# Optimization experiments

Measured on AMD Instinct MI355X. Metric: run time of the kernel, lower is better.

The kernel has to match this reference:

```python
import jax, jax.numpy as jnp
import numpy as np

B, S, E, H, L, NQ, FFN, V, C = 16, 2048, 256, 4, 2, 8, 512, 50257, 2
DK = E // H  # wires per attention head


def _pos_encoding(seq_len, dim):
    pos = jnp.arange(seq_len, dtype=jnp.float32)[:, None]
    div = jnp.exp(jnp.arange(0, dim, 2, dtype=jnp.float32) * (-np.log(10000.0) / dim))
    pe = jnp.zeros((seq_len, dim), dtype=jnp.float32)
    pe = pe.at[:, 0::2].set(jnp.sin(pos * div))
    pe = pe.at[:, 1::2].set(jnp.cos(pos * div))
    return pe


def _layernorm(x, g, b, eps=1e-5):
    m = x.mean(-1, keepdims=True)
    v = ((x - m) ** 2).mean(-1, keepdims=True)
    return (x - m) / jnp.sqrt(v + eps) * g + b


def setup_inputs() -> dict:
    key = jax.random.key(0)
    ks = jax.random.split(key, 9)
    f = lambda k, shape, s: jax.random.normal(k, shape, dtype=jnp.float32) * s
    return {
        "tokens": jax.random.randint(ks[0], (B, S), 0, V),
        "embed": f(ks[1], (V, E), 0.02),
        "attn_theta": f(ks[2], (L, DK), 1.0),
        "combine_w": f(ks[3], (L, E, E), 0.05),
        "combine_b": jnp.zeros((L, E), jnp.float32),
        "ffn_theta": f(ks[4], (L, NQ), 1.0),
        "lin1_w": f(ks[5], (L, NQ, FFN), 0.1),
        "lin1_b": jnp.zeros((L, FFN), jnp.float32),
        "lin2_w": f(ks[6], (L, FFN, E), 0.05),
        "lin2_b": jnp.zeros((L, E), jnp.float32),
        "ln1_g": jnp.ones((L, E), jnp.float32),
        "ln1_b": jnp.zeros((L, E), jnp.float32),
        "ln2_g": jnp.ones((L, E), jnp.float32),
        "ln2_b": jnp.zeros((L, E), jnp.float32),
        "cls_w": f(ks[7], (E, C), 0.05),
        "cls_b": jnp.zeros((C,), jnp.float32),
    }


def reference(tokens, embed, attn_theta, combine_w, combine_b, ffn_theta,
              lin1_w, lin1_b, lin2_w, lin2_b, ln1_g, ln1_b, ln2_g, ln2_b,
              cls_w, cls_b):
    # token embedding + sinusoidal positional encoding
    x = embed[tokens] + _pos_encoding(S, E)[None]  # [B,S,E]
    for l in range(L):
        # QuantumAttention: per-head RX-encode(x) then trainable RX(theta),
        # PauliZ expectation => cos(x + theta); same theta shared across heads,
        # head split/merge preserves feature layout => tile theta over heads.
        theta = jnp.tile(attn_theta[l], H)  # [E]
        attn = jnp.einsum('bse,ef->bsf', jnp.cos(x + theta), combine_w[l]) + combine_b[l]
        x = _layernorm(x + attn, ln1_g[l], ln1_b[l])
        # FeedForwardQuantum: RX-encode first NQ features, trainable RY(theta),
        # PauliZ expectation => cos(x) * cos(theta)
        q = jnp.cos(x[..., :NQ]) * jnp.cos(ffn_theta[l])  # [B,S,NQ]
        h = jax.nn.relu(jnp.einsum('bsn,nf->bsf', q, lin1_w[l]) + lin1_b[l])
        ffn = jnp.einsum('bsf,fe->bse', h, lin2_w[l]) + lin2_b[l]
        x = _layernorm(x + ffn, ln2_g[l], ln2_b[l])
    pooled = x.mean(axis=1)  # [B,E]
    return pooled @ cls_w + cls_b  # [B,C] logits
```

## Files before the change

kernel.cpp:

```cpp
#include <hip/hip_runtime.h>
#include <cstdint>
#include <cstddef>

#define SEQ   2048
#define EDIM  256
#define FFND  512
#define NBATCH 16
#define XLD   264

typedef unsigned short u16;
typedef __attribute__((ext_vector_type(8))) __bf16 bf16x8;
typedef __attribute__((ext_vector_type(4))) float f32x4;

__device__ __forceinline__ float bf2f(u16 u) {
  union { unsigned int w; float f; } v; v.w = ((unsigned int)u) << 16; return v.f;
}
__device__ __forceinline__ u16 f2bf(float f) {
  union { float f; unsigned int w; } v; v.f = f;
  unsigned int r = v.w + 0x7fffu + ((v.w >> 16) & 1u);
  return (u16)(r >> 16);
}
__device__ __forceinline__ float fast_cos(float x) {
  float r = x * 0.15915494309189535f;
  r = r - floorf(r);
  return __builtin_amdgcn_cosf(r);
}
__device__ __forceinline__ void unpack8(bf16x8 v, float* o) {
  const u16* p = (const u16*)&v;
  #pragma unroll
  for (int j = 0; j < 8; ++j) o[j] = bf2f(p[j]);
}

__global__ void sniff_kernel(const void* embed, int* flag) {
  int t = threadIdx.x;
  const u16* p = (const u16*)embed;
  int c = 0;
  #pragma unroll
  for (int j = 0; j < 8; ++j) {
    u16 v = p[t * 8 + j];
    int e = (v >> 7) & 0xff;
    c += (e > 128) ? 1 : 0;
  }
  #pragma unroll
  for (int d = 1; d < 64; d <<= 1) c += __shfl_xor(c, d);
  if (t == 0) *flag = (c > 64) ? 1 : 0;
}

struct CanonArgs { const void* p[14]; };

__global__ void canon_kernel(CanonArgs a, const int* __restrict__ flag, u16* __restrict__ dst) {
  const int off[15] = {0, 128, 131200, 131712, 131728, 139920, 140944, 403088,
                       403600, 404112, 404624, 405136, 405648, 406160, 406162};
  int i = blockIdx.x * 256 + threadIdx.x;
  if (i >= 406162) return;
  int isf32 = *flag;
  int s = 0;
  #pragma unroll
  for (int k = 0; k < 13; ++k) s += (i >= off[k + 1]) ? 1 : 0;
  int j = i - off[s];
  u16 v = isf32 ? f2bf(((const float*)a.p[s])[j]) : ((const u16*)a.p[s])[j];
  dst[i] = v;
}

__global__ void prep_kernel(const u16* __restrict__ cw, const u16* __restrict__ l2,
                            u16* __restrict__ cwT, u16* __restrict__ l2T) {
  int id = blockIdx.x * 256 + threadIdx.x;
  if (id < 2 * 256 * 256) {
    int l = id >> 16, rem = id & 65535;
    int kc = rem >> 11, n = (rem >> 3) & 255, kj = rem & 7;
    cwT[id] = cw[l * 65536 + (kc * 8 + kj) * 256 + n];
  } else {
    int j = id - 131072;
    if (j < 2 * 512 * 256) {
      int l = j >> 17, rem = j & 131071;
      int kc = rem >> 11, n = (rem >> 3) & 255, kj = rem & 7;
      l2T[j] = l2[l * 131072 + (kc * 8 + kj) * 256 + n];
    }
  }
}

__launch_bounds__(256, 2)
__global__ void mega_kernel(const int* __restrict__ tokens, const void* __restrict__ embed,
                            const int* __restrict__ flag, const u16* __restrict__ canon,
                            const u16* __restrict__ cwT, const u16* __restrict__ l2T,
                            float* __restrict__ pooled) {
  __shared__ u16 xt[64 * XLD];
  __shared__ union {
    struct { u16 Bt[256 * 64]; u16 At[64 * 64]; u16 qs[64 * 8]; } k;
    struct { float2 sstat[64][5]; float2 sms[64]; } ln;
  } sh;
  __shared__ u16 thL[64];

  const int tid = threadIdx.x;
  const int wave = tid >> 6, lane = tid & 63;
  const int fr = lane & 15, fq = lane >> 4;
  const int m0 = blockIdx.x * 64;
  const int isf32 = *flag;

  int cols[4];
  #pragma unroll
  for (int ni = 0; ni < 4; ++ni) cols[ni] = wave * 64 + ni * 16 + fr;

  {
    const float c0 = 9.210340371976184f / 128.f;
    const float inv2pi = 0.15915494309189535f;
    #pragma unroll
    for (int it = 0; it < 8; ++it) {
      int c = it * 256 + tid;
      int r = c >> 5, e8 = c & 31;
      int tok = tokens[m0 + r];
      float ev[8];
      if (isf32) {
        const float* ep = (const float*)embed + (size_t)tok * EDIM + e8 * 8;
        float4 a = *(const float4*)ep, b = *(const float4*)(ep + 4);
        ev[0]=a.x; ev[1]=a.y; ev[2]=a.z; ev[3]=a.w; ev[4]=b.x; ev[5]=b.y; ev[6]=b.z; ev[7]=b.w;
      } else {
        const u16* ep = (const u16*)embed + (size_t)tok * EDIM + e8 * 8;
        uint4 v = *(const uint4*)ep;
        unpack8(*(const bf16x8*)&v, ev);
      }
      int s = (m0 + r) & (SEQ - 1);
      u16 o[8];
      #pragma unroll
      for (int j = 0; j < 8; ++j) {
        int e = e8 * 8 + j, i = e >> 1;
        float rev = (float)s * (__expf(-(float)i * c0) * inv2pi);
        rev = rev - floorf(rev);
        float pe = (e & 1) ? __builtin_amdgcn_cosf(rev) : __builtin_amdgcn_sinf(rev);
        o[j] = f2bf(ev[j] + pe);
      }
      *(uint4*)(xt + r * XLD + e8 * 8) = *(const uint4*)o;
    }
  }
  __syncthreads();

  f32x4 acc[4][4];

  auto mfma_step = [&]() {
    const bf16x8* Av = (const bf16x8*)sh.k.At;
    const bf16x8* Bv = (const bf16x8*)sh.k.Bt;
    #pragma unroll
    for (int ks = 0; ks < 2; ++ks) {
      const int kc = ks * 4 + fq;
      bf16x8 af[4], bfv[4];
      #pragma unroll
      for (int mi = 0; mi < 4; ++mi) af[mi] = Av[kc * 64 + ((mi * 16 + fr) ^ kc)];
      #pragma unroll
      for (int ni = 0; ni < 4; ++ni) bfv[ni] = Bv[kc * 256 + cols[ni]];
      #pragma unroll
      for (int mi = 0; mi < 4; ++mi)
        #pragma unroll
        for (int ni = 0; ni < 4; ++ni)
          acc[mi][ni] = __builtin_amdgcn_mfma_f32_16x16x32_bf16(af[mi], bfv[ni], acc[mi][ni], 0, 0, 0);
    }
  };

  auto epilogue = [&](const u16* bias, const u16* gamma, const u16* beta) {
    float bcol[4];
    #pragma unroll
    for (int ni = 0; ni < 4; ++ni) bcol[ni] = bf2f(bias[cols[ni]]);
    #pragma unroll
    for (int mi = 0; mi < 4; ++mi)
      #pragma unroll
      for (int rg = 0; rg < 4; ++rg) {
        int lrow = mi * 16 + fq * 4 + rg;
        #pragma unroll
        for (int ni = 0; ni < 4; ++ni)
          acc[mi][ni][rg] += bf2f(xt[lrow * XLD + cols[ni]]) + bcol[ni];
      }
    float sr[4][4], sq[4][4];
    #pragma unroll
    for (int mi = 0; mi < 4; ++mi)
      #pragma unroll
      for (int rg = 0; rg < 4; ++rg) {
        float a = 0.f, b = 0.f;
        #pragma unroll
        for (int ni = 0; ni < 4; ++ni) { float t2 = acc[mi][ni][rg]; a += t2; b += t2 * t2; }
        sr[mi][rg] = a; sq[mi][rg] = b;
      }
    #pragma unroll
    for (int d = 1; d < 16; d <<= 1)
      #pragma unroll
      for (int mi = 0; mi < 4; ++mi)
        #pragma unroll
        for (int rg = 0; rg < 4; ++rg) {
          sr[mi][rg] += __shfl_xor(sr[mi][rg], d);
          sq[mi][rg] += __shfl_xor(sq[mi][rg], d);
        }
    if (fr == 0) {
      #pragma unroll
      for (int mi = 0; mi < 4; ++mi)
        #pragma unroll
        for (int rg = 0; rg < 4; ++rg)
          sh.ln.sstat[mi * 16 + fq * 4 + rg][wave] = float2{sr[mi][rg], sq[mi][rg]};
    }
    __syncthreads();
    if (tid < 64) {
      float s = 0.f, s2 = 0.f;
      #pragma unroll
      for (int w = 0; w < 4; ++w) { float2 p = sh.ln.sstat[tid][w]; s += p.x; s2 += p.y; }
      float mean = s * (1.f / 256.f);
      float var = fmaxf(s2 * (1.f / 256.f) - mean * mean, 0.f);
      sh.ln.sms[tid] = float2{mean, rsqrtf(var + 1e-5f)};
    }
    __syncthreads();
    float gcol[4], btc[4];
    #pragma unroll
    for (int ni = 0; ni < 4; ++ni) { gcol[ni] = bf2f(gamma[cols[ni]]); btc[ni] = bf2f(beta[cols[ni]]); }
    #pragma unroll
    for (int mi = 0; mi < 4; ++mi)
      #pragma unroll
      for (int rg = 0; rg < 4; ++rg) {
        int lrow = mi * 16 + fq * 4 + rg;
        float2 ms = sh.ln.sms[lrow];
        #pragma unroll
        for (int ni = 0; ni < 4; ++ni) {
          float o = (acc[mi][ni][rg] - ms.x) * ms.y * gcol[ni] + btc[ni];
          xt[lrow * XLD + cols[ni]] = f2bf(o);
        }
      }
    __syncthreads();
  };

  for (int l = 0; l < 2; ++l) {
    if (tid < 8) ((uint4*)thL)[tid] = ((const uint4*)(canon + l * 64))[tid];
    __syncthreads();
    #pragma unroll
    for (int i = 0; i < 4; ++i)
      #pragma unroll
      for (int j = 0; j < 4; ++j) acc[i][j] = {0.f, 0.f, 0.f, 0.f};
    {
      const u16* Bbase = cwT + l * 65536;
      for (int k0 = 0; k0 < 256; k0 += 64) {
        const u16* bsrc = Bbase + (k0 >> 3) * 2048;
        #pragma unroll
        for (int it = 0; it < 8; ++it) {
          int c = tid + it * 256;
          __builtin_amdgcn_global_load_lds(
              (const __attribute__((address_space(1))) void*)(bsrc + (size_t)c * 8),
              (__attribute__((address_space(3))) void*)(sh.k.Bt + c * 8), 16, 0, 0);
        }
        #pragma unroll
        for (int it = 0; it < 2; ++it) {
          int c = it * 256 + tid;
          int f8 = c >> 6, r = c & 63;
          uint4 g = *(const uint4*)(xt + r * XLD + k0 + f8 * 8);
          u16* gp = (u16*)&g;
          #pragma unroll
          for (int j = 0; j < 8; ++j)
            gp[j] = f2bf(fast_cos(bf2f(gp[j]) + bf2f(thL[f8 * 8 + j])));
          ((uint4*)sh.k.At)[f8 * 64 + (r ^ f8)] = g;
        }
        __syncthreads();
        mfma_step();
        __syncthreads();
      }
    }
    epilogue(canon + 131200 + l * 256, canon + 403600 + l * 256, canon + 404112 + l * 256);

    #pragma unroll
    for (int rep = 0; rep < 2; ++rep) {
      int idx = tid + rep * 256;
      int r = idx >> 3, n = idx & 7;
      float cth = fast_cos(bf2f(canon[131712 + l * 8 + n]));
      sh.k.qs[r * 8 + n] = f2bf(fast_cos(bf2f(xt[r * XLD + n])) * cth);
    }
    __syncthreads();

    #pragma unroll
    for (int i = 0; i < 4; ++i)
      #pragma unroll
      for (int j = 0; j < 4; ++j) acc[i][j] = {0.f, 0.f, 0.f, 0.f};
    {
      const u16* B2 = l2T + l * 131072;
      const u16* w1 = canon + 131728 + l * 4096;
      const u16* b1 = canon + 139920 + l * 512;
      for (int k0 = 0; k0 < 512; k0 += 64) {
        const u16* bsrc = B2 + (k0 >> 3) * 2048;
        #pragma unroll
        for (int it = 0; it < 8; ++it) {
          int c = tid + it * 256;
          __builtin_amdgcn_global_load_lds(
              (const __attribute__((address_space(1))) void*)(bsrc + (size_t)c * 8),
              (__attribute__((address_space(3))) void*)(sh.k.Bt + c * 8), 16, 0, 0);
        }
        #pragma unroll
        for (int it = 0; it < 2; ++it) {
          int c = it * 256 + tid;
          int kc = c >> 6, r = c & 63;
          int cc = (k0 >> 3) + kc;
          float qf[8], hv[8];
          unpack8(((const bf16x8*)sh.k.qs)[r], qf);
          { uint4 bv = *(const uint4*)(b1 + cc * 8); unpack8(*(const bf16x8*)&bv, hv); }
          #pragma unroll
          for (int n = 0; n < 8; ++n) {
            uint4 wv = *(const uint4*)(w1 + n * 512 + cc * 8);
            float wf[8];
            unpack8(*(const bf16x8*)&wv, wf);
            #pragma unroll
            for (int j = 0; j < 8; ++j) hv[j] += qf[n] * wf[j];
          }
          uint4 g; u16* gp = (u16*)&g;
          #pragma unroll
          for (int j = 0; j < 8; ++j) gp[j] = f2bf(fmaxf(hv[j], 0.f));
          ((uint4*)sh.k.At)[kc * 64 + (r ^ kc)] = g;
        }
        __syncthreads();
        mfma_step();
        __syncthreads();
      }
    }
    epilogue(canon + 403088 + l * 256, canon + 404624 + l * 256, canon + 405136 + l * 256);
  }

  {
    float s = 0.f;
    #pragma unroll 8
    for (int r = 0; r < 64; ++r) s += bf2f(xt[r * XLD + tid]);
    atomicAdd(&pooled[(m0 >> 11) * EDIM + tid], s);
  }
}

__global__ void logits_kernel(const float* __restrict__ pooled, const u16* __restrict__ clsw,
                              const u16* __restrict__ clsb, const int* __restrict__ flag,
                              void* __restrict__ out) {
  int t = threadIdx.x;
  int b = t >> 4, sub = t & 15;
  float a0 = 0.f, a1 = 0.f;
  #pragma unroll
  for (int j = 0; j < 16; ++j) {
    int e = sub * 16 + j;
    float p = pooled[b * 256 + e];
    a0 += p * bf2f(clsw[e * 2 + 0]);
    a1 += p * bf2f(clsw[e * 2 + 1]);
  }
  #pragma unroll
  for (int d = 1; d < 16; d <<= 1) {
    a0 += __shfl_xor(a0, d);
    a1 += __shfl_xor(a1, d);
  }
  if (sub == 0) {
    float o0 = a0 * (1.f / 2048.f) + bf2f(clsb[0]);
    float o1 = a1 * (1.f / 2048.f) + bf2f(clsb[1]);
    if (*flag) {
      ((float*)out)[b * 2 + 0] = o0; ((float*)out)[b * 2 + 1] = o1;
    } else {
      ((u16*)out)[b * 2 + 0] = f2bf(o0); ((u16*)out)[b * 2 + 1] = f2bf(o1);
    }
  }
}

extern "C" void kernel_launch(void* const* d_in, const int* in_sizes, int n_in,
                              void* d_out, int out_size, void* d_ws, size_t ws_size,
                              hipStream_t stream) {
  const int* tokens = (const int*)d_in[0];

  char* ws = (char*)d_ws;
  u16*   canon  = (u16*)(ws + 0);
  u16*   cwT    = (u16*)(ws + 1048576);
  u16*   l2T    = (u16*)(ws + 1310720);
  float* pooled = (float*)(ws + 1835008);
  int*   flag   = (int*)(ws + 1851392);

  sniff_kernel<<<1, 64, 0, stream>>>(d_in[1], flag);

  CanonArgs ca;
  for (int i = 0; i < 14; ++i) ca.p[i] = d_in[i + 2];
  canon_kernel<<<1587, 256, 0, stream>>>(ca, flag, canon);

  prep_kernel<<<1536, 256, 0, stream>>>(canon + 128, canon + 140944, cwT, l2T);

  hipMemsetAsync(pooled, 0, NBATCH * EDIM * sizeof(float), stream);

  mega_kernel<<<512, 256, 0, stream>>>(tokens, d_in[1], flag, canon, cwT, l2T, pooled);

  logits_kernel<<<1, 256, 0, stream>>>(pooled, canon + 405648, canon + 406160, flag, d_out);
}
```

Before: 215.4 us.

## Run FFN lin1 on MFMA, precompute positional table, simplify LayerNorm reduction

The scalar FMA loop that computed the lin1 hidden activations is replaced by bf16 MFMA with zero-padded K, using q fragments and a transposed lin1 weight produced in the prep kernel. The positional encoding is now computed once by a separate kernel into a workspace table and read in the embedding stage, which removes the per-element exp and sin/cos work. The LayerNorm row statistics now write per-lane partials to shared memory instead of doing shuffle reductions, and one thread per row sums them. In exchange the MFMA wastes three quarters of its K lanes, the scattered 16-bit stores into At may cause bank conflicts, and the positional table adds 2 MB of global reads.

```diff
diff --git a/kernel.cpp b/kernel.cpp
--- a/kernel.cpp
+++ b/kernel.cpp
@@ -63,31 +63,47 @@
 }
 
 __global__ void prep_kernel(const u16* __restrict__ cw, const u16* __restrict__ l2,
-                            u16* __restrict__ cwT, u16* __restrict__ l2T) {
+                            const u16* __restrict__ w1, u16* __restrict__ cwT,
+                            u16* __restrict__ l2T, u16* __restrict__ w1T) {
   int id = blockIdx.x * 256 + threadIdx.x;
-  if (id < 2 * 256 * 256) {
+  if (id < 131072) {
     int l = id >> 16, rem = id & 65535;
     int kc = rem >> 11, n = (rem >> 3) & 255, kj = rem & 7;
     cwT[id] = cw[l * 65536 + (kc * 8 + kj) * 256 + n];
-  } else {
+  } else if (id < 393216) {
     int j = id - 131072;
-    if (j < 2 * 512 * 256) {
-      int l = j >> 17, rem = j & 131071;
-      int kc = rem >> 11, n = (rem >> 3) & 255, kj = rem & 7;
-      l2T[j] = l2[l * 131072 + (kc * 8 + kj) * 256 + n];
-    }
-  }
+    int l = j >> 17, rem = j & 131071;
+    int kc = rem >> 11, n = (rem >> 3) & 255, kj = rem & 7;
+    l2T[j] = l2[l * 131072 + (kc * 8 + kj) * 256 + n];
+  } else if (id < 401408) {
+    int j = id - 393216;
+    int l = j >> 12, rem = j & 4095;
+    int c = rem >> 3, n = rem & 7;
+    w1T[j] = w1[l * 4096 + n * 512 + c];
+  }
+}
+
+__global__ void pe_kernel(float* __restrict__ pe) {
+  int id = blockIdx.x * 256 + threadIdx.x;
+  int s = id >> 8, e = id & 255;
+  const float c0 = 9.210340371976184f / 128.f;
+  const float inv2pi = 0.15915494309189535f;
+  int i = e >> 1;
+  float rev = (float)s * (__expf(-(float)i * c0) * inv2pi);
+  rev = rev - floorf(rev);
+  pe[id] = (e & 1) ? __builtin_amdgcn_cosf(rev) : __builtin_amdgcn_sinf(rev);
 }
 
 __launch_bounds__(256, 2)
 __global__ void mega_kernel(const int* __restrict__ tokens, const void* __restrict__ embed,
                             const int* __restrict__ flag, const u16* __restrict__ canon,
                             const u16* __restrict__ cwT, const u16* __restrict__ l2T,
+                            const u16* __restrict__ w1T, const float* __restrict__ pe,
                             float* __restrict__ pooled) {
   __shared__ u16 xt[64 * XLD];
   __shared__ union {
     struct { u16 Bt[256 * 64]; u16 At[64 * 64]; u16 qs[64 * 8]; } k;
-    struct { float2 sstat[64][5]; float2 sms[64]; } ln;
+    struct { float2 part[64][65]; float2 ms[64]; } ln;
   } sh;
   __shared__ u16 thL[64];
 
@@ -101,36 +117,29 @@
   #pragma unroll
   for (int ni = 0; ni < 4; ++ni) cols[ni] = wave * 64 + ni * 16 + fr;
 
-  {
-    const float c0 = 9.210340371976184f / 128.f;
-    const float inv2pi = 0.15915494309189535f;
-    #pragma unroll
-    for (int it = 0; it < 8; ++it) {
-      int c = it * 256 + tid;
-      int r = c >> 5, e8 = c & 31;
-      int tok = tokens[m0 + r];
-      float ev[8];
-      if (isf32) {
-        const float* ep = (const float*)embed + (size_t)tok * EDIM + e8 * 8;
-        float4 a = *(const float4*)ep, b = *(const float4*)(ep + 4);
-        ev[0]=a.x; ev[1]=a.y; ev[2]=a.z; ev[3]=a.w; ev[4]=b.x; ev[5]=b.y; ev[6]=b.z; ev[7]=b.w;
-      } else {
-        const u16* ep = (const u16*)embed + (size_t)tok * EDIM + e8 * 8;
-        uint4 v = *(const uint4*)ep;
-        unpack8(*(const bf16x8*)&v, ev);
-      }
-      int s = (m0 + r) & (SEQ - 1);
-      u16 o[8];
-      #pragma unroll
-      for (int j = 0; j < 8; ++j) {
-        int e = e8 * 8 + j, i = e >> 1;
-        float rev = (float)s * (__expf(-(float)i * c0) * inv2pi);
-        rev = rev - floorf(rev);
-        float pe = (e & 1) ? __builtin_amdgcn_cosf(rev) : __builtin_amdgcn_sinf(rev);
-        o[j] = f2bf(ev[j] + pe);
-      }
-      *(uint4*)(xt + r * XLD + e8 * 8) = *(const uint4*)o;
-    }
+  #pragma unroll
+  for (int it = 0; it < 8; ++it) {
+    int c = it * 256 + tid;
+    int r = c >> 5, e8 = c & 31;
+    int tok = tokens[m0 + r];
+    float ev[8];
+    if (isf32) {
+      const float* ep = (const float*)embed + (size_t)tok * EDIM + e8 * 8;
+      float4 a = *(const float4*)ep, b = *(const float4*)(ep + 4);
+      ev[0]=a.x; ev[1]=a.y; ev[2]=a.z; ev[3]=a.w; ev[4]=b.x; ev[5]=b.y; ev[6]=b.z; ev[7]=b.w;
+    } else {
+      const u16* ep = (const u16*)embed + (size_t)tok * EDIM + e8 * 8;
+      uint4 v = *(const uint4*)ep;
+      unpack8(*(const bf16x8*)&v, ev);
+    }
+    int s = (m0 + r) & (SEQ - 1);
+    const float* pp = pe + s * EDIM + e8 * 8;
+    float4 p0 = *(const float4*)pp, p1 = *(const float4*)(pp + 4);
+    float pv[8] = {p0.x, p0.y, p0.z, p0.w, p1.x, p1.y, p1.z, p1.w};
+    u16 o[8];
+    #pragma unroll
+    for (int j = 0; j < 8; ++j) o[j] = f2bf(ev[j] + pv[j]);
+    *(uint4*)(xt + r * XLD + e8 * 8) = *(const uint4*)o;
   }
   __syncthreads();
 
@@ -164,44 +173,26 @@
       #pragma unroll
       for (int rg = 0; rg < 4; ++rg) {
         int lrow = mi * 16 + fq * 4 + rg;
-        #pragma unroll
-        for (int ni = 0; ni < 4; ++ni)
-          acc[mi][ni][rg] += bf2f(xt[lrow * XLD + cols[ni]]) + bcol[ni];
-      }
-    float sr[4][4], sq[4][4];
-    #pragma unroll
-    for (int mi = 0; mi < 4; ++mi)
-      #pragma unroll
-      for (int rg = 0; rg < 4; ++rg) {
         float a = 0.f, b = 0.f;
         #pragma unroll
-        for (int ni = 0; ni < 4; ++ni) { float t2 = acc[mi][ni][rg]; a += t2; b += t2 * t2; }
-        sr[mi][rg] = a; sq[mi][rg] = b;
-      }
-    #pragma unroll
-    for (int d = 1; d < 16; d <<= 1)
-      #pragma unroll
-      for (int mi = 0; mi < 4; ++mi)
-        #pragma unroll
-        for (int rg = 0; rg < 4; ++rg) {
-          sr[mi][rg] += __shfl_xor(sr[mi][rg], d);
-          sq[mi][rg] += __shfl_xor(sq[mi][rg], d);
-        }
-    if (fr == 0) {
-      #pragma unroll
-      for (int mi = 0; mi < 4; ++mi)
-        #pragma unroll
-        for (int rg = 0; rg < 4; ++rg)
-          sh.ln.sstat[mi * 16 + fq * 4 + rg][wave] = float2{sr[mi][rg], sq[mi][rg]};
-    }
+        for (int ni = 0; ni < 4; ++ni) {
+          float t2 = acc[mi][ni][rg] + bf2f(xt[lrow * XLD + cols[ni]]) + bcol[ni];
+          acc[mi][ni][rg] = t2;
+          a += t2; b += t2 * t2;
+        }
+        sh.ln.part[lrow][wave * 16 + fr] = float2{a, b};
+      }
     __syncthreads();
     if (tid < 64) {
       float s = 0.f, s2 = 0.f;
       #pragma unroll
-      for (int w = 0; w < 4; ++w) { float2 p = sh.ln.sstat[tid][w]; s += p.x; s2 += p.y; }
+      for (int f = 0; f < 64; f += 2) {
+        float4 p = *(const float4*)&sh.ln.part[tid][f];
+        s += p.x + p.z; s2 += p.y + p.w;
+      }
       float mean = s * (1.f / 256.f);
       float var = fmaxf(s2 * (1.f / 256.f) - mean * mean, 0.f);
-      sh.ln.sms[tid] = float2{mean, rsqrtf(var + 1e-5f)};
+      sh.ln.ms[tid] = float2{mean, rsqrtf(var + 1e-5f)};
     }
     __syncthreads();
     float gcol[4], btc[4];
@@ -212,7 +203,7 @@
       #pragma unroll
       for (int rg = 0; rg < 4; ++rg) {
         int lrow = mi * 16 + fq * 4 + rg;
-        float2 ms = sh.ln.sms[lrow];
+        float2 ms = sh.ln.ms[lrow];
         #pragma unroll
         for (int ni = 0; ni < 4; ++ni) {
           float o = (acc[mi][ni][rg] - ms.x) * ms.y * gcol[ni] + btc[ni];
@@ -267,13 +258,21 @@
     }
     __syncthreads();
 
+    bf16x8 af_q[4];
+    #pragma unroll
+    for (int mi = 0; mi < 4; ++mi) {
+      uint4 qv = {0u, 0u, 0u, 0u};
+      if (fq == 0) qv = *(const uint4*)(sh.k.qs + (mi * 16 + fr) * 8);
+      af_q[mi] = *(const bf16x8*)&qv;
+    }
+
     #pragma unroll
     for (int i = 0; i < 4; ++i)
       #pragma unroll
       for (int j = 0; j < 4; ++j) acc[i][j] = {0.f, 0.f, 0.f, 0.f};
     {
       const u16* B2 = l2T + l * 131072;
-      const u16* w1 = canon + 131728 + l * 4096;
+      const u16* w1t = w1T + l * 4096;
       const u16* b1 = canon + 139920 + l * 512;
       for (int k0 = 0; k0 < 512; k0 += 64) {
         const u16* bsrc = B2 + (k0 >> 3) * 2048;
@@ -284,27 +283,33 @@
               (const __attribute__((address_space(1))) void*)(bsrc + (size_t)c * 8),
               (__attribute__((address_space(3))) void*)(sh.k.Bt + c * 8), 16, 0, 0);
         }
-        #pragma unroll
-        for (int it = 0; it < 2; ++it) {
-          int c = it * 256 + tid;
-          int kc = c >> 6, r = c & 63;
-          int cc = (k0 >> 3) + kc;
-          float qf[8], hv[8];
-          unpack8(((const bf16x8*)sh.k.qs)[r], qf);
-          { uint4 bv = *(const uint4*)(b1 + cc * 8); unpack8(*(const bf16x8*)&bv, hv); }
+        f32x4 acc2[4][4];
+        #pragma unroll
+        for (int ni = 0; ni < 4; ++ni) {
+          float b1v = bf2f(b1[k0 + ni * 16 + fr]);
           #pragma unroll
-          for (int n = 0; n < 8; ++n) {
-            uint4 wv = *(const uint4*)(w1 + n * 512 + cc * 8);
-            float wf[8];
-            unpack8(*(const bf16x8*)&wv, wf);
+          for (int mi = 0; mi < 4; ++mi) acc2[mi][ni] = {b1v, b1v, b1v, b1v};
+        }
+        #pragma unroll
+        for (int ni = 0; ni < 4; ++ni) {
+          uint4 wv = {0u, 0u, 0u, 0u};
+          if (fq == 0) wv = *(const uint4*)(w1t + (size_t)(k0 + ni * 16 + fr) * 8);
+          bf16x8 bfw = *(const bf16x8*)&wv;
+          #pragma unroll
+          for (int mi = 0; mi < 4; ++mi)
+            acc2[mi][ni] = __builtin_amdgcn_mfma_f32_16x16x32_bf16(af_q[mi], bfw, acc2[mi][ni], 0, 0, 0);
+        }
+        #pragma unroll
+        for (int mi = 0; mi < 4; ++mi)
+          #pragma unroll
+          for (int ni = 0; ni < 4; ++ni) {
+            int kk = ni * 16 + fr, kc = kk >> 3;
             #pragma unroll
-            for (int j = 0; j < 8; ++j) hv[j] += qf[n] * wf[j];
+            for (int rg = 0; rg < 4; ++rg) {
+              int r = mi * 16 + fq * 4 + rg;
+              sh.k.At[(kc * 64 + (r ^ kc)) * 8 + (kk & 7)] = f2bf(fmaxf(acc2[mi][ni][rg], 0.f));
+            }
           }
-          uint4 g; u16* gp = (u16*)&g;
-          #pragma unroll
-          for (int j = 0; j < 8; ++j) gp[j] = f2bf(fmaxf(hv[j], 0.f));
-          ((uint4*)sh.k.At)[kc * 64 + (r ^ kc)] = g;
-        }
         __syncthreads();
         mfma_step();
         __syncthreads();
@@ -359,8 +364,10 @@
   u16*   canon  = (u16*)(ws + 0);
   u16*   cwT    = (u16*)(ws + 1048576);
   u16*   l2T    = (u16*)(ws + 1310720);
-  float* pooled = (float*)(ws + 1835008);
-  int*   flag   = (int*)(ws + 1851392);
+  u16*   w1T    = (u16*)(ws + 1835008);
+  float* pooled = (float*)(ws + 1851392);
+  int*   flag   = (int*)(ws + 1867776);
+  float* pe     = (float*)(ws + 2097152);
 
   sniff_kernel<<<1, 64, 0, stream>>>(d_in[1], flag);
 
@@ -368,11 +375,13 @@
   for (int i = 0; i < 14; ++i) ca.p[i] = d_in[i + 2];
   canon_kernel<<<1587, 256, 0, stream>>>(ca, flag, canon);
 
-  prep_kernel<<<1536, 256, 0, stream>>>(canon + 128, canon + 140944, cwT, l2T);
+  pe_kernel<<<2048, 256, 0, stream>>>(pe);
+  prep_kernel<<<1568, 256, 0, stream>>>(canon + 128, canon + 140944, canon + 131728,
+                                        cwT, l2T, w1T);
 
   hipMemsetAsync(pooled, 0, NBATCH * EDIM * sizeof(float), stream);
 
-  mega_kernel<<<512, 256, 0, stream>>>(tokens, d_in[1], flag, canon, cwT, l2T, pooled);
+  mega_kernel<<<512, 256, 0, stream>>>(tokens, d_in[1], flag, canon, cwT, l2T, w1T, pe, pooled);
 
   logits_kernel<<<1, 256, 0, stream>>>(pooled, canon + 405648, canon + 406160, flag, d_out);
 }
```

Measured after the change: 229.2 us. 6.4% more time.
